# Performance work log

Hardware: AMD Instinct MI355X
Metric: run time of the kernel (lower is better)

Reference implementation:

```python
import jax, jax.numpy as jnp
import numpy as np

T, B, E, H = 64, 64, 128, 256
N_ITEMS, N_DATA = 50000, 20000
EPS = 1e-8


def setup_inputs() -> dict:
    key = jax.random.key(0)
    ks = jax.random.split(key, 20)
    lengths = jnp.sort(jax.random.randint(ks[0], (B,), 1, T + 1))[::-1]
    lengths = lengths.at[0].set(T)  # pack_padded_sequence expects max length first
    x = jax.random.randint(ks[1], (T, B), 1, N_ITEMS)
    tmask = jnp.arange(T)[:, None] < lengths[None, :]
    x = jnp.where(tmask, x, 0)  # padding index 0
    s = 0.05
    emb_table = (jax.random.normal(ks[2], (N_ITEMS, E)) * s).at[0].set(0.0)  # padding_idx=0
    data_embeddings = jax.random.normal(ks[3], (N_DATA, E)) * s
    return {
        'x': x, 'lengths': lengths,
        'emb_table': emb_table, 'data_embeddings': data_embeddings,
        'W_ih': jax.random.normal(ks[4], (4 * H, E)) * s,
        'W_hh': jax.random.normal(ks[5], (4 * H, H)) * s,
        'b_ih': jax.random.normal(ks[6], (4 * H,)) * s,
        'b_hh': jax.random.normal(ks[7], (4 * H,)) * s,
        'Wq': jax.random.normal(ks[8], (H, H)) * s, 'bq': jax.random.normal(ks[9], (H,)) * s,
        'Wk': jax.random.normal(ks[10], (H, H)) * s, 'bk': jax.random.normal(ks[11], (H,)) * s,
        'Wv': jax.random.normal(ks[12], (H, H)) * s, 'bv': jax.random.normal(ks[13], (H,)) * s,
        'W_out': jax.random.normal(ks[14], (E, H)) * s, 'b_out': jax.random.normal(ks[15], (E,)) * s,
    }


def _forward(x, lengths, emb_table, data_embeddings, W_ih, W_hh, b_ih, b_hh,
             Wq, bq, Wk, bk, Wv, bv, W_out, b_out):
    t_len, b_sz = x.shape
    e_dim = emb_table.shape[1]
    h_dim = W_hh.shape[1]

    embs0 = emb_table[x]  # (T, B, E); dropout is identity in eval mode
    initial_embs = jax.lax.stop_gradient(embs0)  # .clone().detach() in original

    # PositionalEncoding: original slices by x.size(1) == batch dim (faithful quirk)
    pos = jnp.arange(b_sz, dtype=jnp.float32)[:, None]
    div = jnp.exp(jnp.arange(0, e_dim, 2, dtype=jnp.float32) * (-jnp.log(10000.0) / e_dim))
    enc = jnp.stack([jnp.sin(pos * div), jnp.cos(pos * div)], axis=-1).reshape(b_sz, e_dim)
    embs = embs0 + enc[None, :, :]  # broadcast over time

    # single-layer LSTM over time (gate order i, f, g, o)
    def step(carry, x_t):
        h, c = carry
        gates = x_t @ W_ih.T + h @ W_hh.T + (b_ih + b_hh)  # (B, 4H)
        i, f, g, o = jnp.split(gates, 4, axis=-1)
        c = jax.nn.sigmoid(f) * c + jax.nn.sigmoid(i) * jnp.tanh(g)
        h = jax.nn.sigmoid(o) * jnp.tanh(c)
        return (h, c), h

    h0 = jnp.zeros((b_sz, h_dim), embs.dtype)
    (_, _), lstm_out = jax.lax.scan(step, (h0, h0), embs)  # (T, B, H)

    # pack/pad round-trip zeroes outputs past each length (LSTM is causal)
    tmask = jnp.arange(t_len)[:, None] < lengths[None, :]  # (T, B)
    lstm_out = lstm_out * tmask[:, :, None]
    lstm_out = lstm_out.transpose(1, 0, 2)  # (B, T, H)

    padding_mask = jnp.sum(lstm_out, axis=-1) != 0  # (B, T)

    q = lstm_out @ Wq.T + bq
    k = lstm_out @ Wk.T + bk
    v = lstm_out @ Wv.T + bv
    score = jnp.einsum('bth,bsh->bts', q, k) / jnp.sqrt(jnp.float32(h_dim))
    score = jnp.where(padding_mask[:, None, :], score, -jnp.inf)
    attn = jax.nn.softmax(score, axis=2)
    weighted = jnp.einsum('bts,bsh->bth', attn, v)  # (B, T, H)
    attn_output = jnp.mean(weighted, axis=1) @ W_out.T + b_out  # (B, E)

    # kNN: fused normalize + matmul + argmin + gather over all T at once
    qn = initial_embs / jnp.clip(jnp.linalg.norm(initial_embs, axis=-1, keepdims=True), EPS)
    dn = data_embeddings / jnp.clip(jnp.linalg.norm(data_embeddings, axis=-1, keepdims=True), EPS)
    sims = jnp.einsum('tbe,ne->tbn', qn, dn)  # (T, B, N_DATA)
    idx = jnp.argmax(sims, axis=-1)  # argmin of (1 - sim)
    closest = jnp.mean(data_embeddings[idx], axis=0)  # (B, E)

    attn_output = attn_output * closest
    return attn_output @ emb_table.T  # (B, n_items)


def reference(x, lengths, emb_table, data_embeddings, W_ih, W_hh, b_ih, b_hh,
              Wq, bq, Wk, bk, Wv, bv, W_out, b_out):
    return _forward(x, lengths, emb_table, data_embeddings, W_ih, W_hh, b_ih, b_hh,
                    Wq, bq, Wk, bk, Wv, bv, W_out, b_out)
```

## Files before the change

### kernel.cpp

```cpp
#include <hip/hip_runtime.h>

typedef unsigned int uint;
typedef unsigned short ushort;
typedef unsigned long long u64;

#define NITEMS 50000
#define NDATA  20000
#define BLKCAP 4096u
#define OVCAP  65536u

#define OFF_LSTMOUT   0x0000000ULL
#define OFF_HX        0x0400000ULL
#define OFF_HXM       0x0440000ULL
#define OFF_PACKED    0x0480000ULL
#define OFF_PACKED2   0x0488000ULL
#define OFF_HITCNTS   0x0490000ULL
#define OFF_OHITCNT   0x0490800ULL
#define MEMSET_BYTES  0x0491000ULL
#define OFF_QMARGIN   0x0491000ULL
#define OFF_XW        0x05A0000ULL
#define OFF_QKV       0x15A0000ULL
#define OFF_HITBUF    OFF_QKV
#define OFF_WIHT      0x21A0000ULL
#define OFF_WQKVT     0x2220000ULL
#define OFF_BIASIH    0x22E0000ULL
#define OFF_BQKV      0x22E1000ULL
#define OFF_DNSCALE   0x22E2000ULL
#define OFF_CLOSEST   0x22F6000ULL
#define OFF_AV        0x22FE000ULL
#define OFF_DEMB16    0x2306000ULL
#define OFF_A16       0x27E8000ULL

__device__ __forceinline__ ushort f2bf(float f) {
  union { float f; uint u; } v; v.f = f;
  uint u = v.u;
  return (ushort)((u + 0x7FFFu + ((u >> 16) & 1u)) >> 16);
}
__device__ __forceinline__ uint fkey(float f) {
  union { float f; uint u; } v; v.f = f;
  return (v.u & 0x80000000u) ? ~v.u : (v.u | 0x80000000u);
}
__device__ __forceinline__ u64 shfl_xor_u64(u64 v, int off) {
  uint lo = (uint)v, hi = (uint)(v >> 32);
  lo = (uint)__shfl_xor((int)lo, off);
  hi = (uint)__shfl_xor((int)hi, off);
  return ((u64)hi << 32) | (u64)lo;
}

typedef __attribute__((ext_vector_type(8))) short short8;
typedef __attribute__((ext_vector_type(4))) float floatx4;

#define R32(M) M(0) M(1) M(2) M(3) M(4) M(5) M(6) M(7) M(8) M(9) M(10) M(11) \
  M(12) M(13) M(14) M(15) M(16) M(17) M(18) M(19) M(20) M(21) M(22) M(23) \
  M(24) M(25) M(26) M(27) M(28) M(29) M(30) M(31)

#define HIX(j) ((j) + (((j) >> 7) << 2))

#define LBAR() do { \
  __builtin_amdgcn_sched_barrier(0); \
  asm volatile("s_waitcnt lgkmcnt(0)" ::: "memory"); \
  __builtin_amdgcn_s_barrier(); \
  __builtin_amdgcn_sched_barrier(0); \
} while (0)

__global__ __launch_bounds__(256) void prep_kernel(
    const int* __restrict__ x,
    const float* __restrict__ emb, const float* __restrict__ demb,
    const float* __restrict__ W_ih,
    const float* __restrict__ Wq, const float* __restrict__ Wk, const float* __restrict__ Wv,
    const float* __restrict__ b_ih, const float* __restrict__ b_hh,
    const float* __restrict__ bq, const float* __restrict__ bk, const float* __restrict__ bv,
    float* __restrict__ dnscale, ushort* __restrict__ demb16, ushort* __restrict__ a16,
    float* __restrict__ wiht, float* __restrict__ wqkvt,
    float* __restrict__ biasih, float* __restrict__ bqkv,
    float* __restrict__ qmargin, u64* __restrict__ packed2)
{
  int blk = blockIdx.x, tid = threadIdx.x;
  if (blk < 5000) {
    int row = blk * 4 + (tid >> 6);
    int lane = tid & 63;
    float2 d = *(const float2*)(demb + (size_t)row * 128 + lane * 2);
    float s = d.x * d.x + d.y * d.y;
    for (int off = 32; off; off >>= 1) s += __shfl_xor(s, off);
    if (lane == 0) dnscale[row] = 1.0f / fmaxf(sqrtf(s), 1e-8f);
  } else if (blk < 6250) {
    size_t base = ((size_t)(blk - 5000) * 256 + tid) * 8;
    float4 f1 = *(const float4*)(demb + base);
    float4 f2 = *(const float4*)(demb + base + 4);
    uint4 o;
    o.x = (uint)f2bf(f1.x) | ((uint)f2bf(f1.y) << 16);
    o.y = (uint)f2bf(f1.z) | ((uint)f2bf(f1.w) << 16);
    o.z = (uint)f2bf(f2.x) | ((uint)f2bf(f2.y) << 16);
    o.w = (uint)f2bf(f2.z) | ((uint)f2bf(f2.w) << 16);
    *(uint4*)(demb16 + base) = o;
  } else if (blk < 6506) {
    int idx = (blk - 6250) * 256 + tid;
    int m = idx >> 4, seg = idx & 15;
    const float* src = emb + (size_t)x[m] * 128 + seg * 8;
    float4 f1 = *(const float4*)(src);
    float4 f2 = *(const float4*)(src + 4);
    uint4 o;
    o.x = (uint)f2bf(f1.x) | ((uint)f2bf(f1.y) << 16);
    o.y = (uint)f2bf(f1.z) | ((uint)f2bf(f1.w) << 16);
    o.z = (uint)f2bf(f2.x) | ((uint)f2bf(f2.y) << 16);
    o.w = (uint)f2bf(f2.z) | ((uint)f2bf(f2.w) << 16);
    *(uint4*)(a16 + (size_t)m * 128 + seg * 8) = o;
  } else if (blk < 7018) {
    int f = (blk - 6506) * 256 + tid;
    int r = f >> 7, e = f & 127;
    wiht[e * 1024 + r] = W_ih[f];
  } else if (blk < 7786) {
    int f = (blk - 7018) * 256 + tid;
    int w = f >> 16; int rem = f & 65535;
    int r = rem >> 8, e = rem & 255;
    const float* src = (w == 0) ? Wq : (w == 1) ? Wk : Wv;
    wqkvt[e * 768 + w * 256 + r] = src[rem];
  } else if (blk < 7790) {
    int idx = (blk - 7786) * 256 + tid;
    if (idx < 1024) biasih[idx] = b_ih[idx] + b_hh[idx];
  } else if (blk < 7793) {
    int idx = (blk - 7790) * 256 + tid;
    if (idx < 768) {
      int w = idx >> 8; int r = idx & 255;
      const float* src = (w == 0) ? bq : (w == 1) ? bk : bv;
      bqkv[idx] = src[r];
    }
  } else {
    int row = (blk - 7793) * 4 + (tid >> 6);
    int lane = tid & 63;
    float2 d = *(const float2*)(emb + (size_t)x[row] * 128 + lane * 2);
    float s = d.x * d.x + d.y * d.y;
    for (int off = 32; off; off >>= 1) s += __shfl_xor(s, off);
    if (lane == 0) {
      if (s == 0.f) {
        qmargin[row] = -1e30f;
        packed2[row] = ((u64)fkey(0.0f) << 32) | 0xFFFFFFFFull;
      } else {
        qmargin[row] = 0.017f * sqrtf(s) + 1e-5f;
      }
    }
  }
}

__global__ __launch_bounds__(256) void xw_kernel(
    const int* __restrict__ x, const float* __restrict__ emb,
    const float* __restrict__ wiht, const float* __restrict__ biasih,
    float* __restrict__ xW)
{
  __shared__ __align__(16) float At[128 * 16];
  int blk = blockIdx.x, tid = threadIdx.x;
  int m0 = blk * 16;
  for (int c = 0; c < 8; ++c) {
    int idx = c * 256 + tid;
    int mm = idx >> 7, e = idx & 127;
    int m = m0 + mm;
    int bcol = m & 63;
    int xv = x[m];
    float val = emb[(size_t)xv * 128 + e];
    int j = e >> 1;
    float arg = (float)bcol * __expf((float)j * -0.14391157f);
    val += (e & 1) ? cosf(arg) : sinf(arg);
    At[e * 16 + mm] = val;
  }
  __syncthreads();
  int quad = tid >> 6, l = tid & 63;
  for (int rp = 0; rp < 4; ++rp) {
    int r = rp * 256 + l * 4;
    float acc[4][4] = {};
    for (int e = 0; e < 128; ++e) {
      float4 wv4 = *(const float4*)(wiht + e * 1024 + r);
      float4 av4 = *(const float4*)(At + e * 16 + quad * 4);
      float am[4] = {av4.x, av4.y, av4.z, av4.w};
      float wr4[4] = {wv4.x, wv4.y, wv4.z, wv4.w};
      #pragma unroll
      for (int mi = 0; mi < 4; ++mi)
        #pragma unroll
        for (int ri = 0; ri < 4; ++ri)
          acc[mi][ri] += am[mi] * wr4[ri];
    }
    float4 bv4 = *(const float4*)(biasih + r);
    #pragma unroll
    for (int mi = 0; mi < 4; ++mi) {
      size_t m = (size_t)(m0 + quad * 4 + mi);
      float4 o;
      o.x = acc[mi][0] + bv4.x; o.y = acc[mi][1] + bv4.y;
      o.z = acc[mi][2] + bv4.z; o.w = acc[mi][3] + bv4.w;
      *(float4*)(xW + m * 1024 + r) = o;
    }
  }
}

__global__ __launch_bounds__(256) void knn_kernel(
    const ushort* __restrict__ a16, const ushort* __restrict__ demb16,
    const float* __restrict__ dnscale, const float* __restrict__ qmargin,
    u64* __restrict__ packed, uint* __restrict__ hitcnts, uint* __restrict__ ohitcnt,
    uint* __restrict__ hitbuf)
{
  __shared__ __align__(16) ushort b_sh[2][64 * 144];
  __shared__ uint lcnt;
  int blk = blockIdx.x, tid = threadIdx.x;
  int chunk = blk & 15, mt = blk >> 4;
  int wv = tid >> 6, lane = tid & 63;
  int col = lane & 15, quad = lane >> 4;
  int M0 = mt * 128;
  if (tid == 0) lcnt = 0;
  short8 afrag[2][4];
  #pragma unroll
  for (int s = 0; s < 2; ++s) {
    int mrow = M0 + s * 64 + wv * 16 + col;
    #pragma unroll
    for (int kf = 0; kf < 4; ++kf)
      afrag[s][kf] = *(const short8*)(a16 + (size_t)mrow * 128 + kf * 32 + quad * 8);
  }
  float best[2][4] = {{-1e30f,-1e30f,-1e30f,-1e30f},{-1e30f,-1e30f,-1e30f,-1e30f}};
  int bidx[2][4] = {};
  int nbase = chunk * 1250, nend = nbase + 1250;
  const int niter = 20;
  int srow = tid >> 4, sseg = tid & 15;
  uint4 stg[4]; float scr[4];

  #pragma unroll
  for (int p = 0; p < 4; ++p) {
    int n = nbase + p * 16 + srow;
    uint4 v = {0u,0u,0u,0u};
    if (n < nend) v = *(const uint4*)(demb16 + (size_t)n * 128 + sseg * 8);
    stg[p] = v;
  }
  #pragma unroll
  for (int ns = 0; ns < 4; ++ns) {
    int n = nbase + ns * 16 + col;
    scr[ns] = (n < nend) ? dnscale[n] : 0.f;
  }
  for (int it = 0; it < niter; ++it) {
    int n0 = nbase + it * 64;
    ushort* bsh = b_sh[it & 1];
    #pragma unroll
    for (int p = 0; p < 4; ++p)
      *(uint4*)(&bsh[(p * 16 + srow) * 144 + sseg * 8]) = stg[p];
    float mysc[4] = {scr[0], scr[1], scr[2], scr[3]};
    __syncthreads();
    if (it + 1 < niter) {
      int nb = n0 + 64;
      #pragma unroll
      for (int p = 0; p < 4; ++p) {
        int n = nb + p * 16 + srow;
        uint4 v = {0u,0u,0u,0u};
        if (n < nend) v = *(const uint4*)(demb16 + (size_t)n * 128 + sseg * 8);
        stg[p] = v;
      }
      #pragma unroll
      for (int ns = 0; ns < 4; ++ns) {
        int n = nb + ns * 16 + col;
        scr[ns] = (n < nend) ? dnscale[n] : 0.f;
      }
    }
    #pragma unroll
    for (int ns = 0; ns < 4; ++ns) {
      short8 bfr[4];
      #pragma unroll
      for (int kf = 0; kf < 4; ++kf)
        bfr[kf] = *(const short8*)(&bsh[(ns * 16 + col) * 144 + kf * 32 + quad * 8]);
      int n = n0 + ns * 16 + col;
      float sc = mysc[ns];
      bool valid = (n < nend);
      #pragma unroll
      for (int s = 0; s < 2; ++s) {
        floatx4 acc = {0.f, 0.f, 0.f, 0.f};
        #pragma unroll
        for (int kf = 0; kf < 4; ++kf)
          acc = __builtin_amdgcn_mfma_f32_16x16x32_bf16(afrag[s][kf], bfr[kf], acc, 0, 0, 0);
        #pragma unroll
        for (int r = 0; r < 4; ++r) {
          float sim = acc[r] * sc;
          if (valid && sim > best[s][r]) { best[s][r] = sim; bidx[s][r] = n; }
        }
      }
    }
  }
  float thr[2][4];
  #pragma unroll
  for (int s = 0; s < 2; ++s)
    #pragma unroll
    for (int r = 0; r < 4; ++r) {
      u64 p = ((u64)fkey(best[s][r]) << 32) | (u64)(0xFFFFFFFFu - (uint)bidx[s][r]);
      #pragma unroll
      for (int off = 1; off < 16; off <<= 1) {
        u64 o = shfl_xor_u64(p, off);
        if (o > p) p = o;
      }
      int m = M0 + s * 64 + wv * 16 + quad * 4 + r;
      union { uint u; float f; } bu;
      uint k = (uint)(p >> 32);
      bu.u = (k & 0x80000000u) ? (k & 0x7FFFFFFFu) : ~k;
      thr[s][r] = bu.f - qmargin[m];
      if (col == 0)
        atomicMax((unsigned long long*)&packed[m], (unsigned long long)p);
    }
  __syncthreads();

  uint* myregion = hitbuf + (size_t)blk * BLKCAP;
  uint* ovregion = hitbuf + (size_t)512 * BLKCAP;
  #pragma unroll
  for (int p = 0; p < 4; ++p) {
    int n = nbase + p * 16 + srow;
    uint4 v = {0u,0u,0u,0u};
    if (n < nend) v = *(const uint4*)(demb16 + (size_t)n * 128 + sseg * 8);
    stg[p] = v;
  }
  #pragma unroll
  for (int ns = 0; ns < 4; ++ns) {
    int n = nbase + ns * 16 + col;
    scr[ns] = (n < nend) ? dnscale[n] : 0.f;
  }
  for (int it = 0; it < niter; ++it) {
    int n0 = nbase + it * 64;
    ushort* bsh = b_sh[it & 1];
    #pragma unroll
    for (int p = 0; p < 4; ++p)
      *(uint4*)(&bsh[(p * 16 + srow) * 144 + sseg * 8]) = stg[p];
    float mysc[4] = {scr[0], scr[1], scr[2], scr[3]};
    __syncthreads();
    if (it + 1 < niter) {
      int nb = n0 + 64;
      #pragma unroll
      for (int p = 0; p < 4; ++p) {
        int n = nb + p * 16 + srow;
        uint4 v = {0u,0u,0u,0u};
        if (n < nend) v = *(const uint4*)(demb16 + (size_t)n * 128 + sseg * 8);
        stg[p] = v;
      }
      #pragma unroll
      for (int ns = 0; ns < 4; ++ns) {
        int n = nb + ns * 16 + col;
        scr[ns] = (n < nend) ? dnscale[n] : 0.f;
      }
    }
    #pragma unroll
    for (int ns = 0; ns < 4; ++ns) {
      short8 bfr[4];
      #pragma unroll
      for (int kf = 0; kf < 4; ++kf)
        bfr[kf] = *(const short8*)(&bsh[(ns * 16 + col) * 144 + kf * 32 + quad * 8]);
      int n = n0 + ns * 16 + col;
      float sc = mysc[ns];
      bool valid = (n < nend);
      #pragma unroll
      for (int s = 0; s < 2; ++s) {
        floatx4 acc = {0.f, 0.f, 0.f, 0.f};
        #pragma unroll
        for (int kf = 0; kf < 4; ++kf)
          acc = __builtin_amdgcn_mfma_f32_16x16x32_bf16(afrag[s][kf], bfr[kf], acc, 0, 0, 0);
        #pragma unroll
        for (int r = 0; r < 4; ++r) {
          float sim = acc[r] * sc;
          bool hit = valid && (sim >= thr[s][r]);
          u64 mask = __ballot(hit);
          if (mask) {
            uint lcntv = (uint)__popcll(mask);
            int leader = __ffsll((unsigned long long)mask) - 1;
            uint base = 0;
            if (lane == leader) base = atomicAdd(&lcnt, lcntv);
            base = (uint)__shfl((int)base, leader);
            if (hit) {
              uint pos = base + (uint)__popcll(mask & ((1ull << lane) - 1ull));
              uint mm = (uint)(M0 + s * 64 + wv * 16 + quad * 4 + r);
              uint rec = (mm << 15) | (uint)n;
              if (pos < BLKCAP) {
                myregion[pos] = rec;
              } else {
                uint op = atomicAdd(ohitcnt, 1u);
                if (op < OVCAP) ovregion[op] = rec;
              }
            }
          }
        }
      }
    }
  }
  __syncthreads();
  if (tid == 0) hitcnts[blk] = lcnt;
}

__global__ __launch_bounds__(256) void rescore_kernel(
    const uint* __restrict__ hitbuf, const uint* __restrict__ hitcnts,
    const uint* __restrict__ ohitcnt, const u64* __restrict__ packed,
    const int* __restrict__ x, const float* __restrict__ emb,
    const float* __restrict__ demb, const float* __restrict__ dnscale,
    u64* __restrict__ packed2)
{
  int blk = blockIdx.x, tid = threadIdx.x;
  uint gid = blk * 256 + tid;
  if (gid < 4096) {
    uint m = gid;
    uint n = 0xFFFFFFFFu - (uint)(packed[m] & 0xFFFFFFFFull);
    if (n < NDATA) {
      const float* q = emb + (size_t)x[m] * 128;
      const float* d = demb + (size_t)n * 128;
      double p = 0.0;
      #pragma unroll 8
      for (int e = 0; e < 128; e += 2) {
        float2 qv = *(const float2*)(q + e);
        float2 dv = *(const float2*)(d + e);
        p += (double)qv.x * (double)dv.x + (double)qv.y * (double)dv.y;
      }
      float sx = (float)(p * (double)dnscale[n]);
      u64 key = ((u64)fkey(sx) << 32) | (u64)(0xFFFFFFFFu - n);
      atomicMax((unsigned long long*)&packed2[m], (unsigned long long)key);
    }
  }
  const uint* src; uint cnt; uint stride;
  if (blk < 512) {
    src = hitbuf + (size_t)blk * BLKCAP;
    cnt = hitcnts[blk]; if (cnt > BLKCAP) cnt = BLKCAP;
    stride = 256;
  } else {
    src = hitbuf + (size_t)512 * BLKCAP;
    cnt = *ohitcnt; if (cnt > OVCAP) cnt = OVCAP;
    stride = 16 * 256;
  }
  uint start = (blk < 512) ? tid : (uint)((blk - 512) * 256 + tid);
  for (uint h = start; h < cnt; h += stride) {
    uint rec = src[h];
    uint m = rec >> 15, n = rec & 0x7FFFu;
    if (m >= 4096 || n >= NDATA) continue;
    const float* q = emb + (size_t)x[m] * 128;
    const float* d = demb + (size_t)n * 128;
    double p = 0.0;
    #pragma unroll 8
    for (int e = 0; e < 128; e += 2) {
      float2 qv = *(const float2*)(q + e);
      float2 dv = *(const float2*)(d + e);
      p += (double)qv.x * (double)dv.x + (double)qv.y * (double)dv.y;
    }
    float sx = (float)(p * (double)dnscale[n]);
    u64 key = ((u64)fkey(sx) << 32) | (u64)(0xFFFFFFFFu - n);
    atomicMax((unsigned long long*)&packed2[m], (unsigned long long)key);
  }
}

__global__ __launch_bounds__(512, 2) void lstm_kernel(
    const int* __restrict__ lengths, const float* __restrict__ Whh,
    const float* __restrict__ xW, float* __restrict__ lstm_out,
    u64* __restrict__ hx, u64* __restrict__ hxm)
{
  __shared__ __align__(16) float h_sh[264];
  __shared__ float part_sh[256];
  int blk = blockIdx.x, tid = threadIdx.x;
  int b = blk & 63, q = blk >> 6;
  int row_local = tid >> 1, half = tid & 1;
  int gate = row_local >> 6, jloc = row_local & 63;
  int grow = gate * 256 + q * 64 + jloc;
  const float4* wp4 = (const float4*)(Whh + (size_t)grow * 256 + half * 128);
#define WDECL(i) float4 tt##i = wp4[i]; \
  float w##i##x = tt##i.x, w##i##y = tt##i.y, w##i##z = tt##i.z, w##i##w = tt##i.w;
  R32(WDECL)
#define WPIN(i) asm volatile("" : "+v"(w##i##x), "+v"(w##i##y), "+v"(w##i##z), "+v"(w##i##w));
  R32(WPIN)
  int len = lengths[b];
  if (tid < 256) h_sh[HIX(tid)] = 0.f;
  float cval = 0.f;
  int prm = tid - 320;
  int jr = (prm < q * 64) ? prm : prm + 64;
  bool fast_ok = true;
  int j1 = q * 64 + (tid - 64);
  float xw0 = 0.f, xw1 = 0.f, xw2 = 0.f, xw3 = 0.f;
  if (tid < 64) {
    const float* xwrow = xW + ((size_t)0 * 64 + b) * 1024 + q * 64 + tid;
    xw0 = xwrow[0]; xw1 = xwrow[256]; xw2 = xwrow[512]; xw3 = xwrow[768];
  }
  __syncthreads();
  for (int t = 0; t < len; ++t) {
    float nx0 = 0.f, nx1 = 0.f, nx2 = 0.f, nx3 = 0.f;
    if (tid < 64 && t + 1 < len) {
      const float* xwrow = xW + ((size_t)(t + 1) * 64 + b) * 1024 + q * 64 + tid;
      nx0 = xwrow[0]; nx1 = xwrow[256]; nx2 = xwrow[512]; nx3 = xwrow[768];
    }
    float hprev = 0.f;
    if (tid >= 64 && tid < 128 && t > 0) hprev = h_sh[HIX(j1)];
    const float4* h4 = (const float4*)(h_sh + half * 132);
    float a[4] = {0.f, 0.f, 0.f, 0.f};
#define WACC(i) { float4 hv_ = h4[i]; \
    a[(i) & 3] += w##i##x * hv_.x + w##i##y * hv_.y + w##i##z * hv_.z + w##i##w * hv_.w; }
    R32(WACC)
    float acc = (a[0] + a[2]) + (a[1] + a[3]);
    acc += __shfl_xor(acc, 1);
    if (!half) part_sh[row_local] = acc;
    LBAR();
    if (tid < 64) {
      float gi = part_sh[tid]       + xw0;
      float gf = part_sh[64 + tid]  + xw1;
      float gg = part_sh[128 + tid] + xw2;
      float go = part_sh[192 + tid] + xw3;
      float ii = 1.f / (1.f + __expf(-gi));
      float ff = 1.f / (1.f + __expf(-gf));
      float oo = 1.f / (1.f + __expf(-go));
      float tg = 1.f - 2.f / (1.f + __expf(2.f * gg));
      cval = ff * cval + ii * tg;
      float tc = 1.f - 2.f / (1.f + __expf(2.f * cval));
      float hv = oo * tc;
      int j = q * 64 + tid;
      union { float f; uint u; } cu; cu.f = hv;
      u64 pk = ((u64)cu.u << 32) | (u64)(uint)(t + 1);
      size_t slot = ((size_t)((t + 1) & 1) * 64 + b) * 256 + j;
      __builtin_amdgcn_sched_barrier(0);
      asm volatile("s_waitcnt vmcnt(4)" ::: "memory");
      asm volatile("global_store_dwordx2 %0, %1, off"
                   :: "v"(hxm + slot), "v"(pk) : "memory");
      __hip_atomic_store(hx + slot, pk, __ATOMIC_RELAXED, __HIP_MEMORY_SCOPE_AGENT);
      h_sh[HIX(j)] = hv;
      xw0 = nx0; xw1 = nx1; xw2 = nx2; xw3 = nx3;
    } else if (tid < 128) {
      if (t > 0) lstm_out[((size_t)b * 64 + (t - 1)) * 256 + j1] = hprev;
    } else if (tid >= 320 && t + 1 < len) {
      size_t slot = ((size_t)((t + 1) & 1) * 64 + b) * 256 + jr;
      uint want = (uint)(t + 1);
      u64 v = 0;
      bool got = false;
      if (fast_ok) {
        const u64* ms = hxm + slot;
        for (int tries = 0; tries < 32; ++tries) {
          asm volatile("global_load_dwordx2 %0, %1, off sc0\n\t"
                       "s_waitcnt vmcnt(0)"
                       : "=&v"(v) : "v"(ms) : "memory");
          if ((uint)v == want) { got = true; break; }
        }
        if (!got && t > 0) fast_ok = false;
      }
      if (!got) {
        const u64* as = hx + slot;
        int guard = 0;
        while (true) {
          v = __hip_atomic_load(as, __ATOMIC_RELAXED, __HIP_MEMORY_SCOPE_AGENT);
          if ((uint)v == want || ++guard > (1 << 24)) break;
        }
      }
      union { uint u; float f; } cv; cv.u = (uint)(v >> 32);
      h_sh[HIX(jr)] = cv.f;
    }
    LBAR();
  }
  if (tid >= 64 && tid < 128) {
    float hl = h_sh[HIX(j1)];
    lstm_out[((size_t)b * 64 + (len - 1)) * 256 + j1] = hl;
  }
}

__global__ __launch_bounds__(128) void closest_kernel(
    const u64* __restrict__ packed2, const float* __restrict__ demb,
    float* __restrict__ closest)
{
  int b = blockIdx.x, tid = threadIdx.x;
  float s = 0.f;
  for (int t = 0; t < 64; ++t) {
    uint low = (uint)(packed2[t * 64 + b] & 0xFFFFFFFFull);
    uint n = 0xFFFFFFFFu - low;
    if (n >= NDATA) n = 0;
    s += demb[(size_t)n * 128 + tid];
  }
  closest[b * 128 + tid] = s * (1.0f / 64.0f);
}

__global__ __launch_bounds__(256) void qkv_kernel(
    const float* __restrict__ lstm_out, const float* __restrict__ wqkvt,
    const float* __restrict__ bqkv, float* __restrict__ qkv)
{
  __shared__ __align__(16) float At[256 * 16];
  int blk = blockIdx.x, tid = threadIdx.x;
  int m0 = blk * 16;
  for (int c = 0; c < 16; ++c)
    At[tid * 16 + c] = lstm_out[((size_t)m0 + c) * 256 + tid];
  __syncthreads();
  int quad = tid >> 6, l = tid & 63;
  for (int rp = 0; rp < 3; ++rp) {
    int r = rp * 256 + l * 4;
    float acc[4][4] = {};
    for (int e = 0; e < 256; ++e) {
      float4 wv4 = *(const float4*)(wqkvt + (size_t)e * 768 + r);
      float4 av4 = *(const float4*)(At + e * 16 + quad * 4);
      float am[4] = {av4.x, av4.y, av4.z, av4.w};
      float wr4[4] = {wv4.x, wv4.y, wv4.z, wv4.w};
      #pragma unroll
      for (int mi = 0; mi < 4; ++mi)
        #pragma unroll
        for (int ri = 0; ri < 4; ++ri)
          acc[mi][ri] += am[mi] * wr4[ri];
    }
    float4 bv4 = *(const float4*)(bqkv + r);
    #pragma unroll
    for (int mi = 0; mi < 4; ++mi) {
      size_t m = (size_t)(m0 + quad * 4 + mi);
      float4 o;
      o.x = acc[mi][0] + bv4.x; o.y = acc[mi][1] + bv4.y;
      o.z = acc[mi][2] + bv4.z; o.w = acc[mi][3] + bv4.w;
      *(float4*)(qkv + m * 768 + r) = o;
    }
  }
}

__global__ __launch_bounds__(256) void attn_kernel(
    const float* __restrict__ qkv, const int* __restrict__ lengths,
    const float* __restrict__ closest, const float* __restrict__ W_out,
    const float* __restrict__ b_out, float* __restrict__ av)
{
  __shared__ float k_sh[64 * 257];
  __shared__ __align__(16) float q_sh[4 * 256];
  __shared__ float wpart[4 * 64];
  __shared__ float wtot[64];
  __shared__ float out_sh[256];
  int b = blockIdx.x, tid = threadIdx.x;
  int wv = tid >> 6, lane = tid & 63;
  int len = lengths[b];
  for (int s = 0; s < 64; ++s)
    k_sh[s * 257 + tid] = qkv[((size_t)b * 64 + s) * 768 + 256 + tid];
  wpart[tid] = 0.f;
  for (int tq = 0; tq < 16; ++tq) {
    __syncthreads();
    #pragma unroll
    for (int c = 0; c < 4; ++c)
      q_sh[c * 256 + tid] = qkv[((size_t)b * 64 + tq * 4 + c) * 768 + tid];
    __syncthreads();
    const float* krow = k_sh + lane * 257;
    const float* qrow = q_sh + wv * 256;
    float sc = 0.f;
    #pragma unroll 8
    for (int h = 0; h < 256; ++h)
      sc += qrow[h] * krow[h];
    sc *= 0.0625f;
    bool vs = (lane < len);
    float scm = vs ? sc : -1e30f;
    float mx = scm;
    for (int off = 32; off; off >>= 1) mx = fmaxf(mx, __shfl_xor(mx, off));
    float e = vs ? __expf(sc - mx) : 0.f;
    float sum = e;
    for (int off = 32; off; off >>= 1) sum += __shfl_xor(sum, off);
    wpart[wv * 64 + lane] += e / sum;
  }
  __syncthreads();
  if (tid < 64)
    wtot[tid] = (wpart[tid] + wpart[64 + tid] + wpart[128 + tid] + wpart[192 + tid]) * (1.0f / 64.0f);
  __syncthreads();
  {
    float acc = 0.f;
    for (int s = 0; s < 64; ++s)
      acc += wtot[s] * qkv[((size_t)b * 64 + s) * 768 + 512 + tid];
    out_sh[tid] = acc;
  }
  __syncthreads();
  if (tid < 128) {
    const float4* wr = (const float4*)(W_out + (size_t)tid * 256);
    float p = b_out[tid];
    #pragma unroll
    for (int c = 0; c < 64; ++c) {
      float4 u = wr[c];
      p += out_sh[c * 4 + 0] * u.x + out_sh[c * 4 + 1] * u.y
         + out_sh[c * 4 + 2] * u.z + out_sh[c * 4 + 3] * u.w;
    }
    av[tid * 64 + b] = p * closest[b * 128 + tid];
  }
}

__global__ __launch_bounds__(256) void final_kernel(
    const float* __restrict__ emb, const float* __restrict__ av,
    float* __restrict__ out)
{
  int i = blockIdx.x * 256 + threadIdx.x;
  if (i >= NITEMS) return;
  const float4* row = (const float4*)(emb + (size_t)i * 128);
  float acc[64];
  #pragma unroll
  for (int bb = 0; bb < 64; ++bb) acc[bb] = 0.f;
  for (int e4 = 0; e4 < 32; ++e4) {
    float4 u = row[e4];
    float wvv[4] = {u.x, u.y, u.z, u.w};
    const float* ab = av + e4 * 4 * 64;
    #pragma unroll
    for (int j = 0; j < 4; ++j) {
      #pragma unroll
      for (int bb = 0; bb < 64; ++bb)
        acc[bb] += wvv[j] * ab[j * 64 + bb];
    }
  }
  #pragma unroll
  for (int bb = 0; bb < 64; ++bb)
    out[(size_t)bb * NITEMS + i] = acc[bb];
}

extern "C" void kernel_launch(void* const* d_in, const int* in_sizes, int n_in,
                              void* d_out, int out_size, void* d_ws, size_t ws_size,
                              hipStream_t stream)
{
  const int*   x       = (const int*)d_in[0];
  const int*   lengths = (const int*)d_in[1];
  const float* emb     = (const float*)d_in[2];
  const float* demb    = (const float*)d_in[3];
  const float* W_ih    = (const float*)d_in[4];
  const float* W_hh    = (const float*)d_in[5];
  const float* b_ih    = (const float*)d_in[6];
  const float* b_hh    = (const float*)d_in[7];
  const float* Wq      = (const float*)d_in[8];
  const float* bq      = (const float*)d_in[9];
  const float* Wk      = (const float*)d_in[10];
  const float* bk      = (const float*)d_in[11];
  const float* Wv      = (const float*)d_in[12];
  const float* bv      = (const float*)d_in[13];
  const float* W_out   = (const float*)d_in[14];
  const float* b_out   = (const float*)d_in[15];

  char* ws = (char*)d_ws;
  float*  lstm_out = (float*)(ws + OFF_LSTMOUT);
  u64*    hx       = (u64*)(ws + OFF_HX);
  u64*    hxm      = (u64*)(ws + OFF_HXM);
  u64*    packed   = (u64*)(ws + OFF_PACKED);
  u64*    packed2  = (u64*)(ws + OFF_PACKED2);
  uint*   hitcnts  = (uint*)(ws + OFF_HITCNTS);
  uint*   ohitcnt  = (uint*)(ws + OFF_OHITCNT);
  float*  qmargin  = (float*)(ws + OFF_QMARGIN);
  uint*   hitbuf   = (uint*)(ws + OFF_HITBUF);
  float*  xW       = (float*)(ws + OFF_XW);
  float*  qkv      = (float*)(ws + OFF_QKV);
  float*  wiht     = (float*)(ws + OFF_WIHT);
  float*  wqkvt    = (float*)(ws + OFF_WQKVT);
  float*  biasih   = (float*)(ws + OFF_BIASIH);
  float*  bqkv     = (float*)(ws + OFF_BQKV);
  float*  dnscale  = (float*)(ws + OFF_DNSCALE);
  float*  closest  = (float*)(ws + OFF_CLOSEST);
  float*  av       = (float*)(ws + OFF_AV);
  ushort* demb16   = (ushort*)(ws + OFF_DEMB16);
  ushort* a16      = (ushort*)(ws + OFF_A16);

  hipMemsetAsync(d_ws, 0, (size_t)MEMSET_BYTES, stream);

  hipLaunchKernelGGL(prep_kernel, dim3(8817), dim3(256), 0, stream,
                     x, emb, demb, W_ih, Wq, Wk, Wv, b_ih, b_hh, bq, bk, bv,
                     dnscale, demb16, a16, wiht, wqkvt, biasih, bqkv,
                     qmargin, packed2);
  hipLaunchKernelGGL(xw_kernel, dim3(256), dim3(256), 0, stream,
                     x, emb, wiht, biasih, xW);
  hipLaunchKernelGGL(knn_kernel, dim3(512), dim3(256), 0, stream,
                     a16, demb16, dnscale, qmargin, packed, hitcnts, ohitcnt, hitbuf);
  hipLaunchKernelGGL(rescore_kernel, dim3(528), dim3(256), 0, stream,
                     hitbuf, hitcnts, ohitcnt, packed, x, emb, demb, dnscale, packed2);
  hipLaunchKernelGGL(lstm_kernel, dim3(256), dim3(512), 0, stream,
                     lengths, W_hh, xW, lstm_out, hx, hxm);
  hipLaunchKernelGGL(closest_kernel, dim3(64), dim3(128), 0, stream,
                     packed2, demb, closest);
  hipLaunchKernelGGL(qkv_kernel, dim3(256), dim3(256), 0, stream,
                     lstm_out, wqkvt, bqkv, qkv);
  hipLaunchKernelGGL(attn_kernel, dim3(64), dim3(256), 0, stream,
                     qkv, lengths, closest, W_out, b_out, av);
  hipLaunchKernelGGL(final_kernel, dim3(196), dim3(256), 0, stream,
                     emb, av, (float*)d_out);
}
```

Baseline: 599.5 us.

## Remap LSTM threads so gate reduction uses wave shuffles, double-buffer h

Reassigns LSTM threads so that the four gates of each hidden unit sit in the same wavefront. The gate values can then be gathered with lane shuffles instead of a shared-memory partial buffer and an extra block barrier. The hidden-state buffer is double-buffered in shared memory, each thread preloads its own xW value, and remote h polling is spread across all waves. Blocks are remapped so the four quarter-blocks of one batch element get nearby block IDs. This removes one barrier per timestep and the lagged lstm_out writeback, at the cost of more scattered xW loads and a different pattern of cross-block polling.

```diff
diff --git a/kernel.cpp b/kernel.cpp
--- a/kernel.cpp
+++ b/kernel.cpp
@@ -443,13 +443,16 @@
     const float* __restrict__ xW, float* __restrict__ lstm_out,
     u64* __restrict__ hx, u64* __restrict__ hxm)
 {
-  __shared__ __align__(16) float h_sh[264];
-  __shared__ float part_sh[256];
-  int blk = blockIdx.x, tid = threadIdx.x;
-  int b = blk & 63, q = blk >> 6;
-  int row_local = tid >> 1, half = tid & 1;
-  int gate = row_local >> 6, jloc = row_local & 63;
+  __shared__ __align__(16) float h_sh[2][264];
+  int B = blockIdx.x, tid = threadIdx.x;
+  int q = (B >> 3) & 3;
+  int b = ((B & 7) << 3) | (B >> 5);
+  int w = tid >> 6, lane = tid & 63;
+  int jloc = (w << 3) | (lane >> 3);
+  int gate = (lane >> 1) & 3;
+  int half = lane & 1;
   int grow = gate * 256 + q * 64 + jloc;
+  int jglob = q * 64 + jloc;
   const float4* wp4 = (const float4*)(Whh + (size_t)grow * 256 + half * 128);
 #define WDECL(i) float4 tt##i = wp4[i]; \
   float w##i##x = tt##i.x, w##i##y = tt##i.y, w##i##z = tt##i.z, w##i##w = tt##i.w;
@@ -457,40 +460,32 @@
 #define WPIN(i) asm volatile("" : "+v"(w##i##x), "+v"(w##i##y), "+v"(w##i##z), "+v"(w##i##w));
   R32(WPIN)
   int len = lengths[b];
-  if (tid < 256) h_sh[HIX(tid)] = 0.f;
+  if (tid < 264) h_sh[0][tid] = 0.f;
+  bool isPub = ((lane & 7) == 0);
+  int rr = w * 24 + lane;
+  int jr = (rr < q * 64) ? rr : rr + 64;
   float cval = 0.f;
-  int prm = tid - 320;
-  int jr = (prm < q * 64) ? prm : prm + 64;
   bool fast_ok = true;
-  int j1 = q * 64 + (tid - 64);
-  float xw0 = 0.f, xw1 = 0.f, xw2 = 0.f, xw3 = 0.f;
-  if (tid < 64) {
-    const float* xwrow = xW + ((size_t)0 * 64 + b) * 1024 + q * 64 + tid;
-    xw0 = xwrow[0]; xw1 = xwrow[256]; xw2 = xwrow[512]; xw3 = xwrow[768];
-  }
+  float xwv = xW[((size_t)0 * 64 + b) * 1024 + grow];
   __syncthreads();
   for (int t = 0; t < len; ++t) {
-    float nx0 = 0.f, nx1 = 0.f, nx2 = 0.f, nx3 = 0.f;
-    if (tid < 64 && t + 1 < len) {
-      const float* xwrow = xW + ((size_t)(t + 1) * 64 + b) * 1024 + q * 64 + tid;
-      nx0 = xwrow[0]; nx1 = xwrow[256]; nx2 = xwrow[512]; nx3 = xwrow[768];
-    }
-    float hprev = 0.f;
-    if (tid >= 64 && tid < 128 && t > 0) hprev = h_sh[HIX(j1)];
-    const float4* h4 = (const float4*)(h_sh + half * 132);
+    float nxw = 0.f;
+    if (t + 1 < len) nxw = xW[((size_t)(t + 1) * 64 + b) * 1024 + grow];
+    const float4* h4 = (const float4*)(&h_sh[t & 1][half * 132]);
     float a[4] = {0.f, 0.f, 0.f, 0.f};
 #define WACC(i) { float4 hv_ = h4[i]; \
     a[(i) & 3] += w##i##x * hv_.x + w##i##y * hv_.y + w##i##z * hv_.z + w##i##w * hv_.w; }
     R32(WACC)
     float acc = (a[0] + a[2]) + (a[1] + a[3]);
     acc += __shfl_xor(acc, 1);
-    if (!half) part_sh[row_local] = acc;
-    LBAR();
-    if (tid < 64) {
-      float gi = part_sh[tid]       + xw0;
-      float gf = part_sh[64 + tid]  + xw1;
-      float gg = part_sh[128 + tid] + xw2;
-      float go = part_sh[192 + tid] + xw3;
+    acc += xwv;
+    int base = lane & ~7;
+    float gi = __shfl(acc, base);
+    float gf = __shfl(acc, base + 2);
+    float gg = __shfl(acc, base + 4);
+    float go = __shfl(acc, base + 6);
+    float* hB = h_sh[(t + 1) & 1];
+    if (isPub) {
       float ii = 1.f / (1.f + __expf(-gi));
       float ff = 1.f / (1.f + __expf(-gf));
       float oo = 1.f / (1.f + __expf(-go));
@@ -498,26 +493,21 @@
       cval = ff * cval + ii * tg;
       float tc = 1.f - 2.f / (1.f + __expf(2.f * cval));
       float hv = oo * tc;
-      int j = q * 64 + tid;
       union { float f; uint u; } cu; cu.f = hv;
       u64 pk = ((u64)cu.u << 32) | (u64)(uint)(t + 1);
-      size_t slot = ((size_t)((t + 1) & 1) * 64 + b) * 256 + j;
-      __builtin_amdgcn_sched_barrier(0);
-      asm volatile("s_waitcnt vmcnt(4)" ::: "memory");
+      size_t slot = ((size_t)((t + 1) & 1) * 64 + b) * 256 + jglob;
       asm volatile("global_store_dwordx2 %0, %1, off"
                    :: "v"(hxm + slot), "v"(pk) : "memory");
       __hip_atomic_store(hx + slot, pk, __ATOMIC_RELAXED, __HIP_MEMORY_SCOPE_AGENT);
-      h_sh[HIX(j)] = hv;
-      xw0 = nx0; xw1 = nx1; xw2 = nx2; xw3 = nx3;
-    } else if (tid < 128) {
-      if (t > 0) lstm_out[((size_t)b * 64 + (t - 1)) * 256 + j1] = hprev;
-    } else if (tid >= 320 && t + 1 < len) {
-      size_t slot = ((size_t)((t + 1) & 1) * 64 + b) * 256 + jr;
+      lstm_out[((size_t)b * 64 + t) * 256 + jglob] = hv;
+      hB[HIX(jglob)] = hv;
+    }
+    if (lane < 24 && t + 1 < len) {
+      size_t rslot = ((size_t)((t + 1) & 1) * 64 + b) * 256 + jr;
       uint want = (uint)(t + 1);
-      u64 v = 0;
-      bool got = false;
+      u64 v = 0; bool got = false;
       if (fast_ok) {
-        const u64* ms = hxm + slot;
+        const u64* ms = hxm + rslot;
         for (int tries = 0; tries < 32; ++tries) {
           asm volatile("global_load_dwordx2 %0, %1, off sc0\n\t"
                        "s_waitcnt vmcnt(0)"
@@ -527,7 +517,7 @@
         if (!got && t > 0) fast_ok = false;
       }
       if (!got) {
-        const u64* as = hx + slot;
+        const u64* as = hx + rslot;
         int guard = 0;
         while (true) {
           v = __hip_atomic_load(as, __ATOMIC_RELAXED, __HIP_MEMORY_SCOPE_AGENT);
@@ -535,13 +525,10 @@
         }
       }
       union { uint u; float f; } cv; cv.u = (uint)(v >> 32);
-      h_sh[HIX(jr)] = cv.f;
-    }
+      hB[HIX(jr)] = cv.f;
+    }
+    xwv = nxw;
     LBAR();
-  }
-  if (tid >= 64 && tid < 128) {
-    float hl = h_sh[HIX(j1)];
-    lstm_out[((size_t)b * 64 + (len - 1)) * 256 + j1] = hl;
   }
 }
 
```

New measurement: 635.6 us. 6.0% more time.

## Fuse hit rescoring into knn kernel and merge qkv with residual rescore

Applied to the files above, without the earlier changes.

Each knn block now rescores its own candidate hits in fp64 at the end of the kernel, so the standalone rescore launch is gone. The per-row argmax rescore and the overflow-hit rescore are folded into a new combined kernel together with the QKV projection. That kernel runs after the LSTM. The overflow buffer moves to its own workspace region, because the hit buffer aliases the qkv output that is now written later. This removes one kernel launch and its global round trip of hit records. In exchange, the knn tail grows longer, and the new offset must fit inside the allocated workspace.

```diff
diff --git a/kernel.cpp b/kernel.cpp
--- a/kernel.cpp
+++ b/kernel.cpp
@@ -30,6 +30,7 @@
 #define OFF_AV        0x22FE000ULL
 #define OFF_DEMB16    0x2306000ULL
 #define OFF_A16       0x27E8000ULL
+#define OFF_OVF       0x28E8000ULL
 
 __device__ __forceinline__ ushort f2bf(float f) {
   union { float f; uint u; } v; v.f = f;
@@ -194,7 +195,9 @@
     const ushort* __restrict__ a16, const ushort* __restrict__ demb16,
     const float* __restrict__ dnscale, const float* __restrict__ qmargin,
     u64* __restrict__ packed, uint* __restrict__ hitcnts, uint* __restrict__ ohitcnt,
-    uint* __restrict__ hitbuf)
+    uint* __restrict__ hitbuf, uint* __restrict__ ovbuf,
+    const int* __restrict__ x, const float* __restrict__ emb,
+    const float* __restrict__ demb, u64* __restrict__ packed2)
 {
   __shared__ __align__(16) ushort b_sh[2][64 * 144];
   __shared__ uint lcnt;
@@ -299,7 +302,7 @@
   __syncthreads();
 
   uint* myregion = hitbuf + (size_t)blk * BLKCAP;
-  uint* ovregion = hitbuf + (size_t)512 * BLKCAP;
+  uint* ovregion = ovbuf;
   #pragma unroll
   for (int p = 0; p < 4; ++p) {
     int n = nbase + p * 16 + srow;
@@ -379,57 +382,18 @@
   }
   __syncthreads();
   if (tid == 0) hitcnts[blk] = lcnt;
-}
-
-__global__ __launch_bounds__(256) void rescore_kernel(
-    const uint* __restrict__ hitbuf, const uint* __restrict__ hitcnts,
-    const uint* __restrict__ ohitcnt, const u64* __restrict__ packed,
-    const int* __restrict__ x, const float* __restrict__ emb,
-    const float* __restrict__ demb, const float* __restrict__ dnscale,
-    u64* __restrict__ packed2)
-{
-  int blk = blockIdx.x, tid = threadIdx.x;
-  uint gid = blk * 256 + tid;
-  if (gid < 4096) {
-    uint m = gid;
-    uint n = 0xFFFFFFFFu - (uint)(packed[m] & 0xFFFFFFFFull);
-    if (n < NDATA) {
-      const float* q = emb + (size_t)x[m] * 128;
-      const float* d = demb + (size_t)n * 128;
-      double p = 0.0;
-      #pragma unroll 8
-      for (int e = 0; e < 128; e += 2) {
-        float2 qv = *(const float2*)(q + e);
-        float2 dv = *(const float2*)(d + e);
-        p += (double)qv.x * (double)dv.x + (double)qv.y * (double)dv.y;
-      }
-      float sx = (float)(p * (double)dnscale[n]);
-      u64 key = ((u64)fkey(sx) << 32) | (u64)(0xFFFFFFFFu - n);
-      atomicMax((unsigned long long*)&packed2[m], (unsigned long long)key);
-    }
-  }
-  const uint* src; uint cnt; uint stride;
-  if (blk < 512) {
-    src = hitbuf + (size_t)blk * BLKCAP;
-    cnt = hitcnts[blk]; if (cnt > BLKCAP) cnt = BLKCAP;
-    stride = 256;
-  } else {
-    src = hitbuf + (size_t)512 * BLKCAP;
-    cnt = *ohitcnt; if (cnt > OVCAP) cnt = OVCAP;
-    stride = 16 * 256;
-  }
-  uint start = (blk < 512) ? tid : (uint)((blk - 512) * 256 + tid);
-  for (uint h = start; h < cnt; h += stride) {
-    uint rec = src[h];
+  uint rcnt = lcnt; if (rcnt > BLKCAP) rcnt = BLKCAP;
+  for (uint h = tid; h < rcnt; h += 256) {
+    uint rec = myregion[h];
     uint m = rec >> 15, n = rec & 0x7FFFu;
     if (m >= 4096 || n >= NDATA) continue;
-    const float* q = emb + (size_t)x[m] * 128;
-    const float* d = demb + (size_t)n * 128;
+    const float* qr = emb + (size_t)x[m] * 128;
+    const float* dr = demb + (size_t)n * 128;
     double p = 0.0;
     #pragma unroll 8
     for (int e = 0; e < 128; e += 2) {
-      float2 qv = *(const float2*)(q + e);
-      float2 dv = *(const float2*)(d + e);
+      float2 qv = *(const float2*)(qr + e);
+      float2 dv = *(const float2*)(dr + e);
       p += (double)qv.x * (double)dv.x + (double)qv.y * (double)dv.y;
     }
     float sx = (float)(p * (double)dnscale[n]);
@@ -545,6 +509,87 @@
   }
 }
 
+__global__ __launch_bounds__(256) void fused_post_kernel(
+    const float* __restrict__ lstm_out, const float* __restrict__ wqkvt,
+    const float* __restrict__ bqkv, float* __restrict__ qkv,
+    const u64* __restrict__ packed, const uint* __restrict__ ohitcnt,
+    const uint* __restrict__ ovbuf, const int* __restrict__ x,
+    const float* __restrict__ emb, const float* __restrict__ demb,
+    const float* __restrict__ dnscale, u64* __restrict__ packed2)
+{
+  __shared__ __align__(16) float At[256 * 16];
+  int blk = blockIdx.x, tid = threadIdx.x;
+  if (blk < 256) {
+    int m0 = blk * 16;
+    for (int c = 0; c < 16; ++c)
+      At[tid * 16 + c] = lstm_out[((size_t)m0 + c) * 256 + tid];
+    __syncthreads();
+    int quad = tid >> 6, l = tid & 63;
+    for (int rp = 0; rp < 3; ++rp) {
+      int r = rp * 256 + l * 4;
+      float acc[4][4] = {};
+      for (int e = 0; e < 256; ++e) {
+        float4 wv4 = *(const float4*)(wqkvt + (size_t)e * 768 + r);
+        float4 av4 = *(const float4*)(At + e * 16 + quad * 4);
+        float am[4] = {av4.x, av4.y, av4.z, av4.w};
+        float wr4[4] = {wv4.x, wv4.y, wv4.z, wv4.w};
+        #pragma unroll
+        for (int mi = 0; mi < 4; ++mi)
+          #pragma unroll
+          for (int ri = 0; ri < 4; ++ri)
+            acc[mi][ri] += am[mi] * wr4[ri];
+      }
+      float4 bv4 = *(const float4*)(bqkv + r);
+      #pragma unroll
+      for (int mi = 0; mi < 4; ++mi) {
+        size_t m = (size_t)(m0 + quad * 4 + mi);
+        float4 o;
+        o.x = acc[mi][0] + bv4.x; o.y = acc[mi][1] + bv4.y;
+        o.z = acc[mi][2] + bv4.z; o.w = acc[mi][3] + bv4.w;
+        *(float4*)(qkv + m * 768 + r) = o;
+      }
+    }
+    return;
+  }
+  if (blk < 272) {
+    uint m = (uint)(blk - 256) * 256 + tid;
+    uint n = 0xFFFFFFFFu - (uint)(packed[m] & 0xFFFFFFFFull);
+    if (n < NDATA) {
+      const float* qr = emb + (size_t)x[m] * 128;
+      const float* dr = demb + (size_t)n * 128;
+      double p = 0.0;
+      #pragma unroll 8
+      for (int e = 0; e < 128; e += 2) {
+        float2 qv = *(const float2*)(qr + e);
+        float2 dv = *(const float2*)(dr + e);
+        p += (double)qv.x * (double)dv.x + (double)qv.y * (double)dv.y;
+      }
+      float sx = (float)(p * (double)dnscale[n]);
+      u64 key = ((u64)fkey(sx) << 32) | (u64)(0xFFFFFFFFu - n);
+      atomicMax((unsigned long long*)&packed2[m], (unsigned long long)key);
+    }
+    return;
+  }
+  uint cnt = *ohitcnt; if (cnt > OVCAP) cnt = OVCAP;
+  for (uint h = (uint)(blk - 272) * 256 + tid; h < cnt; h += 16 * 256) {
+    uint rec = ovbuf[h];
+    uint m = rec >> 15, n = rec & 0x7FFFu;
+    if (m >= 4096 || n >= NDATA) continue;
+    const float* qr = emb + (size_t)x[m] * 128;
+    const float* dr = demb + (size_t)n * 128;
+    double p = 0.0;
+    #pragma unroll 8
+    for (int e = 0; e < 128; e += 2) {
+      float2 qv = *(const float2*)(qr + e);
+      float2 dv = *(const float2*)(dr + e);
+      p += (double)qv.x * (double)dv.x + (double)qv.y * (double)dv.y;
+    }
+    float sx = (float)(p * (double)dnscale[n]);
+    u64 key = ((u64)fkey(sx) << 32) | (u64)(0xFFFFFFFFu - n);
+    atomicMax((unsigned long long*)&packed2[m], (unsigned long long)key);
+  }
+}
+
 __global__ __launch_bounds__(128) void closest_kernel(
     const u64* __restrict__ packed2, const float* __restrict__ demb,
     float* __restrict__ closest)
@@ -558,43 +603,6 @@
     s += demb[(size_t)n * 128 + tid];
   }
   closest[b * 128 + tid] = s * (1.0f / 64.0f);
-}
-
-__global__ __launch_bounds__(256) void qkv_kernel(
-    const float* __restrict__ lstm_out, const float* __restrict__ wqkvt,
-    const float* __restrict__ bqkv, float* __restrict__ qkv)
-{
-  __shared__ __align__(16) float At[256 * 16];
-  int blk = blockIdx.x, tid = threadIdx.x;
-  int m0 = blk * 16;
-  for (int c = 0; c < 16; ++c)
-    At[tid * 16 + c] = lstm_out[((size_t)m0 + c) * 256 + tid];
-  __syncthreads();
-  int quad = tid >> 6, l = tid & 63;
-  for (int rp = 0; rp < 3; ++rp) {
-    int r = rp * 256 + l * 4;
-    float acc[4][4] = {};
-    for (int e = 0; e < 256; ++e) {
-      float4 wv4 = *(const float4*)(wqkvt + (size_t)e * 768 + r);
-      float4 av4 = *(const float4*)(At + e * 16 + quad * 4);
-      float am[4] = {av4.x, av4.y, av4.z, av4.w};
-      float wr4[4] = {wv4.x, wv4.y, wv4.z, wv4.w};
-      #pragma unroll
-      for (int mi = 0; mi < 4; ++mi)
-        #pragma unroll
-        for (int ri = 0; ri < 4; ++ri)
-          acc[mi][ri] += am[mi] * wr4[ri];
-    }
-    float4 bv4 = *(const float4*)(bqkv + r);
-    #pragma unroll
-    for (int mi = 0; mi < 4; ++mi) {
-      size_t m = (size_t)(m0 + quad * 4 + mi);
-      float4 o;
-      o.x = acc[mi][0] + bv4.x; o.y = acc[mi][1] + bv4.y;
-      o.z = acc[mi][2] + bv4.z; o.w = acc[mi][3] + bv4.w;
-      *(float4*)(qkv + m * 768 + r) = o;
-    }
-  }
 }
 
 __global__ __launch_bounds__(256) void attn_kernel(
@@ -716,6 +724,7 @@
   uint*   ohitcnt  = (uint*)(ws + OFF_OHITCNT);
   float*  qmargin  = (float*)(ws + OFF_QMARGIN);
   uint*   hitbuf   = (uint*)(ws + OFF_HITBUF);
+  uint*   ovbuf    = (uint*)(ws + OFF_OVF);
   float*  xW       = (float*)(ws + OFF_XW);
   float*  qkv      = (float*)(ws + OFF_QKV);
   float*  wiht     = (float*)(ws + OFF_WIHT);
@@ -737,15 +746,15 @@
   hipLaunchKernelGGL(xw_kernel, dim3(256), dim3(256), 0, stream,
                      x, emb, wiht, biasih, xW);
   hipLaunchKernelGGL(knn_kernel, dim3(512), dim3(256), 0, stream,
-                     a16, demb16, dnscale, qmargin, packed, hitcnts, ohitcnt, hitbuf);
-  hipLaunchKernelGGL(rescore_kernel, dim3(528), dim3(256), 0, stream,
-                     hitbuf, hitcnts, ohitcnt, packed, x, emb, demb, dnscale, packed2);
+                     a16, demb16, dnscale, qmargin, packed, hitcnts, ohitcnt,
+                     hitbuf, ovbuf, x, emb, demb, packed2);
   hipLaunchKernelGGL(lstm_kernel, dim3(256), dim3(512), 0, stream,
                      lengths, W_hh, xW, lstm_out, hx, hxm);
+  hipLaunchKernelGGL(fused_post_kernel, dim3(288), dim3(256), 0, stream,
+                     lstm_out, wqkvt, bqkv, qkv, packed, ohitcnt, ovbuf,
+                     x, emb, demb, dnscale, packed2);
   hipLaunchKernelGGL(closest_kernel, dim3(64), dim3(128), 0, stream,
                      packed2, demb, closest);
-  hipLaunchKernelGGL(qkv_kernel, dim3(256), dim3(256), 0, stream,
-                     lstm_out, wqkvt, bqkv, qkv);
   hipLaunchKernelGGL(attn_kernel, dim3(64), dim3(256), 0, stream,
                      qkv, lengths, closest, W_out, b_out, av);
   hipLaunchKernelGGL(final_kernel, dim3(196), dim3(256), 0, stream,
```

Result: faster. 584.8 us (-2.4%).
